# Kernel tuning notes

Hardware: AMD Instinct MI355X
Metric: run time of the kernel (lower is better)

## Reference

```python
import jax, jax.numpy as jnp
import numpy as np

P = 100000   # num places
T = 100000   # num transitions
E = 400000   # edges per direction
H = 128      # hidden_dim
L = 3        # num_gnn_layers


def setup_inputs() -> dict:
    key = jax.random.key(0)
    ks = jax.random.split(key, 24)
    w = lambda i, sh: jax.random.normal(ks[i], sh, dtype=jnp.float32) * 0.02
    z = lambda sh: jnp.zeros(sh, dtype=jnp.float32)
    return {
        "place_features": jax.random.uniform(ks[0], (P,), dtype=jnp.float32),
        "transition_features": jax.random.normal(ks[1], (T, 8), dtype=jnp.float32),
        "prefix_encoding": jax.random.normal(ks[2], (18,), dtype=jnp.float32),
        # pre edges: place -> transition ; post edges: transition -> place
        "pre_edge_index": jnp.stack([jax.random.randint(ks[3], (E,), 0, P),
                                     jax.random.randint(ks[4], (E,), 0, T)]).astype(jnp.int32),
        "post_edge_index": jnp.stack([jax.random.randint(ks[5], (E,), 0, T),
                                      jax.random.randint(ks[6], (E,), 0, P)]).astype(jnp.int32),
        # embeddings
        "W_pe": w(7, (1, H)), "b_pe": z((H,)),
        "W_te": w(8, (8, H)), "b_te": z((H,)),
        "W_pr": w(9, (18, H)), "b_pr": z((H,)),
        # per-layer HeteroGraphConv params (stacked over L)
        "p2t_W": w(10, (L, H, H)), "p2t_b": z((L, H)),
        "t2p_W": w(11, (L, H, H)), "t2p_b": z((L, H)),
        "pu_W": w(12, (L, 2 * H, H)), "pu_b": z((L, H)),
        "tu_W": w(13, (L, 2 * H, H)), "tu_b": z((L, H)),
        "pa_W": w(14, (L, H)), "pa_b": z((L,)),
        "ta_W": w(15, (L, H)), "ta_b": z((L,)),
        # pooling + predictor head
        "W_pp": w(16, (H, H)), "b_pp": z((H,)),
        "W_tp": w(17, (H, H)), "b_tp": z((H,)),
        "W1": w(18, (3 * H, 2 * H)), "b1": z((2 * H,)),
        "W2": w(19, (2 * H, H)), "b2": z((H,)),
        "W3": w(20, (H, T)), "b3": z((T,)),
    }


def _forward(place_features, transition_features, prefix_encoding,
             W_pe, b_pe, W_te, b_te, W_pr, b_pr,
             p2t_W, p2t_b, t2p_W, t2p_b, pu_W, pu_b, tu_W, tu_b,
             pa_W, pa_b, ta_W, ta_b,
             W_pp, b_pp, W_tp, b_tp, W1, b1, W2, b2, W3, b3,
             pre_edge_index, post_edge_index):
    place_h = place_features[:, None] @ W_pe + b_pe            # [P,H]
    trans_h = transition_features @ W_te + b_te                # [T,H]
    prefix_h = prefix_encoding[None, :] @ W_pr + b_pr          # [1,H]
    p_src, p_dst = pre_edge_index[0], pre_edge_index[1]        # place idx, trans idx
    t_src, t_dst = post_edge_index[0], post_edge_index[1]      # trans idx, place idx
    nP, nT = place_h.shape[0], trans_h.shape[0]
    for l in range(L):  # fixed small layer count
        # place -> transition: gather, linear, softmax over ALL edges (dim=0 in torch), scatter-add
        m_pt = place_h[p_src] @ p2t_W[l] + p2t_b[l]            # [E,H]
        a_pt = jax.nn.softmax(m_pt @ ta_W[l] + ta_b[l], axis=0)  # [E]
        trans_msg = jax.ops.segment_sum(m_pt * a_pt[:, None], p_dst, num_segments=nT)
        # transition -> place
        m_tp = trans_h[t_src] @ t2p_W[l] + t2p_b[l]            # [E,H]
        a_tp = jax.nn.softmax(m_tp @ pa_W[l] + pa_b[l], axis=0)
        place_msg = jax.ops.segment_sum(m_tp * a_tp[:, None], t_dst, num_segments=nP)
        # residual update + relu (dropout is identity at eval)
        place_new = jnp.concatenate([place_h, place_msg], axis=1) @ pu_W[l] + pu_b[l]
        trans_new = jnp.concatenate([trans_h, trans_msg], axis=1) @ tu_W[l] + tu_b[l]
        place_h = jax.nn.relu(place_h + place_new)
        trans_h = jax.nn.relu(trans_h + trans_new)
    place_global = jnp.mean(place_h @ W_pp + b_pp, axis=0, keepdims=True)   # [1,H]
    trans_global = jnp.mean(trans_h @ W_tp + b_tp, axis=0, keepdims=True)   # [1,H]
    combined = jnp.concatenate([place_global, trans_global, prefix_h], axis=1)  # [1,3H]
    h1 = jax.nn.relu(combined @ W1 + b1)
    h2 = jax.nn.relu(h1 @ W2 + b2)
    logits = h2 @ W3 + b3                                      # [1,T]
    return jax.nn.sigmoid(logits)                              # predicted_transitions


def reference(place_features, transition_features, prefix_encoding,
              pre_edge_index, post_edge_index,
              W_pe, b_pe, W_te, b_te, W_pr, b_pr,
              p2t_W, p2t_b, t2p_W, t2p_b, pu_W, pu_b, tu_W, tu_b,
              pa_W, pa_b, ta_W, ta_b,
              W_pp, b_pp, W_tp, b_tp, W1, b1, W2, b2, W3, b3):
    return _forward(place_features, transition_features, prefix_encoding,
                    W_pe, b_pe, W_te, b_te, W_pr, b_pr,
                    p2t_W, p2t_b, t2p_W, t2p_b, pu_W, pu_b, tu_W, tu_b,
                    pa_W, pa_b, ta_W, ta_b,
                    W_pp, b_pp, W_tp, b_tp, W1, b1, W2, b2, W3, b3,
                    pre_edge_index, post_edge_index)
```

## Files before the change

### kernel.cpp

```cpp
#include <hip/hip_runtime.h>
#include <cstddef>

#define H 128

typedef unsigned short ushort_t;
typedef unsigned char uchar_t;
typedef __attribute__((ext_vector_type(8))) short short8;
typedef __attribute__((ext_vector_type(4))) float floatx4;
typedef __attribute__((ext_vector_type(2))) float floatx2;

__device__ __forceinline__ unsigned fkey(float f){
    unsigned u = __float_as_uint(f);
    return (u & 0x80000000u) ? ~u : (u | 0x80000000u);
}
__device__ __forceinline__ float funkey(unsigned k){
    unsigned u = (k & 0x80000000u) ? (k ^ 0x80000000u) : ~k;
    return __uint_as_float(u);
}
__device__ __forceinline__ ushort_t f2bf(float f){
    unsigned u = __float_as_uint(f);
    u += 0x7fffu + ((u >> 16) & 1u);
    return (ushort_t)(u >> 16);
}
__device__ __forceinline__ float bf2f(ushort_t h){
    return __uint_as_float(((unsigned)h) << 16);
}
__device__ __forceinline__ uchar_t f2fp8(float v){
    int p = __builtin_amdgcn_cvt_pk_fp8_f32(v, v, 0, false);
    return (uchar_t)(p & 0xff);
}
__device__ __forceinline__ void gll16(const void* g, void* l){
    __builtin_amdgcn_global_load_lds(
        (const __attribute__((address_space(1))) unsigned int*)g,
        (__attribute__((address_space(3))) unsigned int*)l, 16, 0, 0);
}
__device__ __forceinline__ void acc8f8(float* a, int2 u, float w){
    floatx2 p;
    p = __builtin_amdgcn_cvt_pk_f32_fp8(u.x, false); a[0] += w*p.x; a[1] += w*p.y;
    p = __builtin_amdgcn_cvt_pk_f32_fp8(u.x, true);  a[2] += w*p.x; a[3] += w*p.y;
    p = __builtin_amdgcn_cvt_pk_f32_fp8(u.y, false); a[4] += w*p.x; a[5] += w*p.y;
    p = __builtin_amdgcn_cvt_pk_f32_fp8(u.y, true);  a[6] += w*p.x; a[7] += w*p.y;
}

__global__ __launch_bounds__(256) void k_embed_place(
    const float* __restrict__ pf, const float* __restrict__ Wpe,
    const float* __restrict__ bpe, ushort_t* __restrict__ out,
    uchar_t* __restrict__ outf8, int P)
{
    int idx = blockIdx.x*256 + threadIdx.x;
    if (idx >= P*32) return;
    int p = idx >> 5, q = (idx & 31) << 2;
    float v = pf[p];
    float4 w = *(const float4*)(Wpe + q);
    float4 b = *(const float4*)(bpe + q);
    float v0 = v*w.x + b.x, v1 = v*w.y + b.y, v2 = v*w.z + b.z, v3 = v*w.w + b.w;
    ushort4 o;
    o.x = f2bf(v0); o.y = f2bf(v1); o.z = f2bf(v2); o.w = f2bf(v3);
    *(ushort4*)(out + (size_t)p*H + q) = o;
    int pk = __builtin_amdgcn_cvt_pk_fp8_f32(v0, v1, 0, false);
    pk = __builtin_amdgcn_cvt_pk_fp8_f32(v2, v3, pk, true);
    *(int*)(outf8 + (size_t)p*H + q) = pk;
}

__global__ __launch_bounds__(256) void k_embed_trans(
    const float* __restrict__ tf, const float* __restrict__ Wte,
    const float* __restrict__ bte, ushort_t* __restrict__ out,
    uchar_t* __restrict__ outf8, int T)
{
    __shared__ float Wl[8*H];
    __shared__ float Bl[H];
    int tid = threadIdx.x;
    #pragma unroll
    for (int t = 0; t < 4; t++) Wl[tid + t*256] = Wte[tid + t*256];
    if (tid < H) Bl[tid] = bte[tid];
    __syncthreads();
    int idx = blockIdx.x*256 + tid;
    if (idx >= T*32) return;
    int t = idx >> 5, q = (idx & 31) << 2;
    float4 acc = *(float4*)(&Bl[q]);
    #pragma unroll
    for (int k = 0; k < 8; k++){
        float s = tf[(size_t)t*8 + k];
        float4 w = *(float4*)(&Wl[k*H + q]);
        acc.x += s*w.x; acc.y += s*w.y; acc.z += s*w.z; acc.w += s*w.w;
    }
    ushort4 o;
    o.x = f2bf(acc.x); o.y = f2bf(acc.y); o.z = f2bf(acc.z); o.w = f2bf(acc.w);
    *(ushort4*)(out + (size_t)t*H + q) = o;
    int pk = __builtin_amdgcn_cvt_pk_fp8_f32(acc.x, acc.y, 0, false);
    pk = __builtin_amdgcn_cvt_pk_fp8_f32(acc.z, acc.w, pk, true);
    *(int*)(outf8 + (size_t)t*H + q) = pk;
}

__global__ void k_init_small(const float* __restrict__ pe, int plen,
                             const float* __restrict__ Wpr, const float* __restrict__ bpr,
                             float* __restrict__ prefix, float* __restrict__ meanP,
                             float* __restrict__ meanT, float* __restrict__ slots)
{
    int c = threadIdx.x;
    float a = bpr[c];
    for (int k = 0; k < plen; k++) a += pe[k]*Wpr[k*H + c];
    prefix[c] = a;
    meanP[c] = 0.f;
    meanT[c] = 0.f;
    if (c < 16) slots[c] = 0.f;
}

__global__ __launch_bounds__(256) void k_wconv(
    const float* __restrict__ tu_W, const float* __restrict__ pu_W,
    ushort_t* __restrict__ WT, int total)
{
    int e = blockIdx.x*256 + threadIdx.x;
    if (e >= total) return;
    int l = e / 32768, oo = e - l*32768;
    int side = oo >> 14, o2 = oo & 16383;
    int n = o2 >> 7, k = o2 & 127;
    const float* Bm = side ? (pu_W + (size_t)l*32768) : (tu_W + (size_t)l*32768);
    WT[(size_t)l*65536 + (size_t)side*32768 + n*256 + k] = f2bf(Bm[(size_t)k*H + n]);
}

__global__ __launch_bounds__(256) void k_wfold(
    const float* __restrict__ p2t_W, const float* __restrict__ t2p_W,
    const float* __restrict__ tu_W,  const float* __restrict__ pu_W,
    ushort_t* __restrict__ WT, int total)
{
    int e = blockIdx.x*256 + threadIdx.x;
    if (e >= total) return;
    int l = e / 32768, oo = e - l*32768;
    int side = oo >> 14, o2 = oo & 16383;
    int n = o2 >> 7, k = o2 & 127;
    const float* A  = side ? (t2p_W + (size_t)l*16384) : (p2t_W + (size_t)l*16384);
    const float* Bm = side ? (pu_W  + (size_t)l*32768) : (tu_W  + (size_t)l*32768);
    const float* Ar = A + (size_t)k*H;
    const float* Bc = Bm + (size_t)128*H + n;
    float s = 0.f;
    #pragma unroll 4
    for (int j = 0; j < 128; j++) s += Ar[j] * Bc[(size_t)j*H];
    WT[(size_t)l*65536 + (size_t)side*32768 + n*256 + 128 + k] = f2bf(s);
}

__global__ __launch_bounds__(128) void k_wsmall(
    const float* __restrict__ p2t_W, const float* __restrict__ t2p_W,
    const float* __restrict__ tu_W,  const float* __restrict__ pu_W,
    const float* __restrict__ p2t_b, const float* __restrict__ t2p_b,
    const float* __restrict__ ta_W,  const float* __restrict__ ta_b,
    const float* __restrict__ pa_W,  const float* __restrict__ pa_b,
    float* __restrict__ wv, float* __restrict__ c0v, float* __restrict__ bcv)
{
    int b = blockIdx.x, l = b >> 1, side = b & 1;
    const float* A  = side ? (t2p_W + (size_t)l*16384) : (p2t_W + (size_t)l*16384);
    const float* Bm = side ? (pu_W  + (size_t)l*32768) : (tu_W  + (size_t)l*32768);
    const float* ab = side ? (t2p_b + (size_t)l*H) : (p2t_b + (size_t)l*H);
    const float* av = side ? (pa_W  + (size_t)l*H) : (ta_W  + (size_t)l*H);
    float asc       = side ? pa_b[l] : ta_b[l];
    int tid = threadIdx.x;
    int o = (l*2 + side)*H;
    float s = 0.f;
    for (int n = 0; n < 128; n++) s += A[(size_t)tid*H + n] * av[n];
    wv[o + tid] = s;
    float s2 = 0.f;
    for (int j = 0; j < 128; j++) s2 += ab[j] * Bm[(size_t)(128+j)*H + tid];
    bcv[o + tid] = s2;
    if (tid == 0){
        float c = 0.f;
        for (int n = 0; n < 128; n++) c += ab[n]*av[n];
        c0v[l*2 + side] = c + asc;
    }
}

__global__ __launch_bounds__(256) void k_zero_ints(int* __restrict__ p, int n)
{
    int i = blockIdx.x*256 + threadIdx.x;
    int stride = gridDim.x*256;
    for (; i < n; i += stride) p[i] = 0;
}

__global__ __launch_bounds__(256) void k_hist2(
    const int* __restrict__ preD, const int* __restrict__ postD, int E,
    int* __restrict__ cntPre, int* __restrict__ cntPost,
    int* __restrict__ rankPre, int* __restrict__ rankPost)
{
    int i = blockIdx.x*256 + threadIdx.x;
    int stride = gridDim.x*256;
    for (; i < E; i += stride){
        rankPre[i] = atomicAdd(&cntPre[preD[i]], 1);
        rankPost[i] = atomicAdd(&cntPost[postD[i]], 1);
    }
}

__global__ __launch_bounds__(256) void k_scan_part(
    const int* __restrict__ cnt, int N, int* __restrict__ bsum)
{
    __shared__ int wsum[4];
    int tid = threadIdx.x, lane = tid & 63, wid = tid >> 6;
    int base = blockIdx.x*1024 + tid*4;
    int4 v = make_int4(0,0,0,0);
    if (base + 3 < N) v = *(const int4*)(cnt + base);
    else {
        if (base+0 < N) v.x = cnt[base+0];
        if (base+1 < N) v.y = cnt[base+1];
        if (base+2 < N) v.z = cnt[base+2];
    }
    int s = v.x + v.y + v.z + v.w;
    #pragma unroll
    for (int o = 1; o < 64; o <<= 1) s += __shfl_xor(s, o);
    if (lane == 0) wsum[wid] = s;
    __syncthreads();
    if (tid == 0) bsum[blockIdx.x] = wsum[0] + wsum[1] + wsum[2] + wsum[3];
}

__global__ __launch_bounds__(256) void k_scan_bsum(int* __restrict__ bsum, int nb)
{
    __shared__ int wsum[4];
    int tid = threadIdx.x, lane = tid & 63, wid = tid >> 6;
    int x = (tid < nb) ? bsum[tid] : 0;
    int inc = x;
    #pragma unroll
    for (int o = 1; o < 64; o <<= 1){
        int u = __shfl_up(inc, o);
        if (lane >= o) inc += u;
    }
    if (lane == 63) wsum[wid] = inc;
    __syncthreads();
    int woff = 0;
    if (wid > 0) woff += wsum[0];
    if (wid > 1) woff += wsum[1];
    if (wid > 2) woff += wsum[2];
    if (tid < nb) bsum[tid] = woff + inc - x;
}

__global__ __launch_bounds__(256) void k_scan_final(
    const int* __restrict__ cnt, int N, const int* __restrict__ bsum,
    int* __restrict__ rp, int E)
{
    __shared__ int wsum[4];
    int tid = threadIdx.x, lane = tid & 63, wid = tid >> 6;
    int base = blockIdx.x*1024 + tid*4;
    int4 v = make_int4(0,0,0,0);
    if (base + 3 < N) v = *(const int4*)(cnt + base);
    else {
        if (base+0 < N) v.x = cnt[base+0];
        if (base+1 < N) v.y = cnt[base+1];
        if (base+2 < N) v.z = cnt[base+2];
    }
    int t0 = v.x, t1 = t0 + v.y, t2 = t1 + v.z, t3 = t2 + v.w;
    int inc = t3;
    #pragma unroll
    for (int o = 1; o < 64; o <<= 1){
        int u = __shfl_up(inc, o);
        if (lane >= o) inc += u;
    }
    if (lane == 63) wsum[wid] = inc;
    __syncthreads();
    int woff = 0;
    if (wid > 0) woff += wsum[0];
    if (wid > 1) woff += wsum[1];
    if (wid > 2) woff += wsum[2];
    int off = bsum[blockIdx.x] + woff + inc - t3;
    if (base+0 < N) rp[base+0] = off;
    if (base+1 < N) rp[base+1] = off + t0;
    if (base+2 < N) rp[base+2] = off + t1;
    if (base+3 < N) rp[base+3] = off + t2;
    if (blockIdx.x == 0 && tid == 0) rp[N] = E;
}

__global__ __launch_bounds__(256) void k_fill2(
    const int* __restrict__ preS, const int* __restrict__ preD,
    const int* __restrict__ postS, const int* __restrict__ postD, int E,
    const int* __restrict__ rpPre, const int* __restrict__ rankPre, int* __restrict__ csrPre,
    const int* __restrict__ rpPost, const int* __restrict__ rankPost, int* __restrict__ csrPost)
{
    int i = blockIdx.x*256 + threadIdx.x;
    int stride = gridDim.x*256;
    for (; i < E; i += stride){
        csrPre[rpPre[preD[i]] + rankPre[i]] = preS[i];
        csrPost[rpPost[postD[i]] + rankPost[i]] = postS[i];
    }
}

__global__ __launch_bounds__(256) void k_gemv(
    const ushort_t* __restrict__ A, int M,
    const float* __restrict__ wv, const float* __restrict__ c0v, int c0i,
    float* __restrict__ y, unsigned* __restrict__ Mkey)
{
    __shared__ float wm[4];
    int tid = threadIdx.x, lane = tid & 63, wid = tid >> 6;
    int g = tid >> 4, gl = tid & 15;
    float w8[8];
    #pragma unroll
    for (int i = 0; i < 8; i++) w8[i] = wv[gl*8 + i];
    float c0 = c0v[c0i];
    int stride = gridDim.x*16;
    float lmax = -3.402823466e38f;
    for (int r = blockIdx.x*16 + g; r < M; r += stride){
        short8 u = *(const short8*)(A + (size_t)r*H + gl*8);
        float s = 0.f;
        #pragma unroll
        for (int i = 0; i < 8; i++) s += bf2f((ushort_t)u[i]) * w8[i];
        s += __shfl_xor(s, 1); s += __shfl_xor(s, 2);
        s += __shfl_xor(s, 4); s += __shfl_xor(s, 8);
        s += c0;
        if (gl == 0) y[r] = s;
        lmax = fmaxf(lmax, s);
    }
    #pragma unroll
    for (int o = 1; o < 64; o <<= 1) lmax = fmaxf(lmax, __shfl_xor(lmax, o));
    if (lane == 0) wm[wid] = lmax;
    __syncthreads();
    if (tid == 0){
        float m = fmaxf(fmaxf(wm[0], wm[1]), fmaxf(wm[2], wm[3]));
        atomicMax(Mkey, fkey(m));
    }
}

__global__ __launch_bounds__(256) void k_sumexp(
    const int* __restrict__ src, int E, const float* __restrict__ y,
    const unsigned* __restrict__ Mkey, float* __restrict__ Sp)
{
    __shared__ float red[4];
    int tid = threadIdx.x, lane = tid & 63, wid = tid >> 6;
    int gid = blockIdx.x*256 + tid, stride = gridDim.x*256;
    float Mv = funkey(Mkey[0]);
    float ls = 0.f;
    for (int e = gid; e < E; e += stride) ls += expf(y[src[e]] - Mv);
    #pragma unroll
    for (int o = 1; o < 64; o <<= 1) ls += __shfl_xor(ls, o);
    if (lane == 0) red[wid] = ls;
    __syncthreads();
    if (tid == 0) atomicAdd(Sp, red[0] + red[1] + red[2] + red[3]);
}

__global__ __launch_bounds__(256) void k_gatherH(
    const int* __restrict__ rp, const int* __restrict__ csr, int Nrow,
    const float* __restrict__ y, const uchar_t* __restrict__ X,
    ushort_t* __restrict__ G, float* __restrict__ sdeg,
    const unsigned* __restrict__ Mkey)
{
    int tid = threadIdx.x;
    int g = tid >> 4, gl = tid & 15;
    int r = blockIdx.x*16 + g;
    if (r >= Nrow) return;
    float Mv = funkey(Mkey[0]);
    int j0 = rp[r], j1 = rp[r+1];
    const int2* X8 = (const int2*)X;
    float a[8] = {0.f,0.f,0.f,0.f,0.f,0.f,0.f,0.f};
    float se = 0.f;
    int j = j0;
    for (; j + 1 < j1; j += 2){
        int s0 = csr[j], s1 = csr[j+1];
        float e0 = expf(y[s0] - Mv);
        float e1 = expf(y[s1] - Mv);
        int2 u0 = X8[(size_t)s0*16 + gl];
        int2 u1 = X8[(size_t)s1*16 + gl];
        se += e0 + e1;
        acc8f8(a, u0, e0);
        acc8f8(a, u1, e1);
    }
    if (j < j1){
        int s0 = csr[j];
        float e0 = expf(y[s0] - Mv);
        int2 u0 = X8[(size_t)s0*16 + gl];
        se += e0;
        acc8f8(a, u0, e0);
    }
    int4 o;
    o.x = (int)((((unsigned)f2bf(a[1])) << 16) | (unsigned)f2bf(a[0]));
    o.y = (int)((((unsigned)f2bf(a[3])) << 16) | (unsigned)f2bf(a[2]));
    o.z = (int)((((unsigned)f2bf(a[5])) << 16) | (unsigned)f2bf(a[4]));
    o.w = (int)((((unsigned)f2bf(a[7])) << 16) | (unsigned)f2bf(a[6]));
    ((int4*)G)[(size_t)r*16 + gl] = o;
    if (gl == 0) sdeg[r] = se;
}

__global__ __launch_bounds__(256, 4) void k_gemm_up(
    const ushort_t* A1, const ushort_t* __restrict__ A2,
    const ushort_t* __restrict__ WT, const float* __restrict__ bias,
    const float* __restrict__ bcp, const float* __restrict__ Sp,
    const float* __restrict__ sdeg,
    ushort_t* out, uchar_t* __restrict__ outF8, int M,
    float* __restrict__ colsum)
{
    __shared__ __align__(16) char As[3*8192];
    __shared__ float csum[H];
    int tid = threadIdx.x;
    int lane = tid & 63, wid = tid >> 6;
    int quad = lane >> 4, l15 = lane & 15;
    int strip = wid*32;
    short8 bfr1[2][4], bfr2[2][4];
    float bcol[2], bc2[2];
    #pragma unroll
    for (int j = 0; j < 2; j++){
        int col = strip + j*16 + l15;
        #pragma unroll
        for (int kk = 0; kk < 4; kk++){
            bfr1[j][kk] = *(const short8*)(WT + (size_t)col*256 + kk*32 + quad*8);
            bfr2[j][kk] = *(const short8*)(WT + (size_t)col*256 + 128 + kk*32 + quad*8);
        }
        bcol[j] = bias[col];
        bc2[j]  = bcp[col];
    }
    short8 If0, If1;
    #pragma unroll
    for (int e = 0; e < 8; e++){
        int kloc = quad*8 + e;
        If0[e] = (kloc == l15)      ? (short)0x3F80 : (short)0;
        If1[e] = (kloc == l15 + 16) ? (short)0x3F80 : (short)0;
    }
    float invS = 1.f / Sp[0];
    const bool has_cs = (colsum != nullptr);
    if (has_cs && tid < H) csum[tid] = 0.f;
    float cs[2] = {0.f, 0.f};

    int tiles = (M + 15) >> 4;
    int G = gridDim.x;
    int t0 = blockIdx.x;
    if (t0 >= tiles) return;
    int srow = tid >> 4;
    int su = (tid & 15) ^ srow;
    const ushort_t* g1b = A1 + (size_t)srow*H + su*8;
    const ushort_t* g2b = A2 + (size_t)srow*H + su*8;
    char* AsB = As;

    #define STAGE_UP(bo, t) do { \
        gll16(g1b + (size_t)(t)*(16*H), AsB + (bo) + (wid<<10)); \
        gll16(g2b + (size_t)(t)*(16*H), AsB + (bo) + 4096 + (wid<<10)); \
    } while(0)

    STAGE_UP(0, t0);
    int t1p = t0 + G;
    if (t1p < tiles){
        STAGE_UP(8192, t1p);
        asm volatile("s_waitcnt vmcnt(2)\ns_barrier" ::: "memory");
    } else {
        asm volatile("s_waitcnt vmcnt(0)\ns_barrier" ::: "memory");
    }

    int t = t0, bo = 0;
    for (;;){
        const char* rb = AsB + bo;
        int row0 = t << 4;
        float4 sd4 = *(const float4*)(sdeg + row0 + quad*4);
        float sdv[4] = {sd4.x, sd4.y, sd4.z, sd4.w};
        short8 a1f[4], a2f[4];
        #pragma unroll
        for (int kk = 0; kk < 4; kk++){
            int sw = ((((kk<<2)+quad) ^ l15) << 4);
            a1f[kk] = *(const short8*)(rb + (l15<<8) + sw);
            a2f[kk] = *(const short8*)(rb + 4096 + (l15<<8) + sw);
        }
        short8 ares = *(const short8*)(rb + (l15<<8) + ((((wid<<2)+quad) ^ l15) << 4));
        floatx4 acc1[2], acc2[2];
        acc1[0] = __builtin_amdgcn_mfma_f32_16x16x32_bf16(ares, If0, (floatx4)0.f, 0,0,0);
        acc1[1] = __builtin_amdgcn_mfma_f32_16x16x32_bf16(ares, If1, (floatx4)0.f, 0,0,0);
        acc2[0] = (floatx4)0.f; acc2[1] = (floatx4)0.f;
        #pragma unroll
        for (int j = 0; j < 2; j++){
            #pragma unroll
            for (int kk = 0; kk < 4; kk++)
                acc1[j] = __builtin_amdgcn_mfma_f32_16x16x32_bf16(a1f[kk], bfr1[j][kk], acc1[j], 0,0,0);
            #pragma unroll
            for (int kk = 0; kk < 4; kk++)
                acc2[j] = __builtin_amdgcn_mfma_f32_16x16x32_bf16(a2f[kk], bfr2[j][kk], acc2[j], 0,0,0);
        }
        #pragma unroll
        for (int j = 0; j < 2; j++){
            int col = strip + j*16 + l15;
            #pragma unroll
            for (int rr = 0; rr < 4; rr++){
                int grow = row0 + quad*4 + rr;
                float v = acc1[j][rr] + invS*(acc2[j][rr] + sdv[rr]*bc2[j]) + bcol[j];
                v = fmaxf(v, 0.f);
                out[(size_t)grow*H + col] = f2bf(v);
                outF8[(size_t)grow*H + col] = f2fp8(v);
                if (has_cs) cs[j] += v;
            }
        }
        int tn = t + G;
        if (tn >= tiles) break;
        int tnn = tn + G;
        int bo2 = bo + 8192; if (bo2 >= 24576) bo2 = 0;
        int bo3 = bo2 + 8192; if (bo3 >= 24576) bo3 = 0;
        if (tnn < tiles){
            STAGE_UP(bo3, tnn);
            asm volatile("s_waitcnt vmcnt(19)\ns_barrier" ::: "memory");
        } else {
            asm volatile("s_waitcnt vmcnt(17)\ns_barrier" ::: "memory");
        }
        t = tn; bo = bo2;
    }
    #undef STAGE_UP
    if (has_cs){
        #pragma unroll
        for (int j = 0; j < 2; j++){
            float v = cs[j];
            v += __shfl_xor(v, 16); v += __shfl_xor(v, 32);
            if (quad == 0) atomicAdd(&csum[strip + j*16 + l15], v);
        }
        __syncthreads();
        if (tid < H) atomicAdd(&colsum[tid], csum[tid]);
    }
}

__global__ __launch_bounds__(256) void k_head(
    const float* __restrict__ meanP, const float* __restrict__ meanT,
    float invP, float invT,
    const float* __restrict__ Wpp, const float* __restrict__ bpp,
    const float* __restrict__ Wtp, const float* __restrict__ btp,
    const float* __restrict__ prefix,
    const float* __restrict__ W1, const float* __restrict__ b1,
    const float* __restrict__ W2, const float* __restrict__ b2,
    float* __restrict__ h2g)
{
    __shared__ float comb[384];
    __shared__ float h1s[256];
    int tid = threadIdx.x;
    if (tid < 128){
        float a = bpp[tid];
        for (int k = 0; k < 128; k++) a += meanP[k]*invP*Wpp[k*H + tid];
        comb[tid] = a;
        comb[256 + tid] = prefix[tid];
    } else {
        int c = tid - 128;
        float a = btp[c];
        for (int k = 0; k < 128; k++) a += meanT[k]*invT*Wtp[k*H + c];
        comb[128 + c] = a;
    }
    __syncthreads();
    {
        float a = b1[tid];
        for (int k = 0; k < 384; k++) a += comb[k]*W1[k*256 + tid];
        h1s[tid] = fmaxf(a, 0.f);
    }
    __syncthreads();
    if (tid < 128){
        float a = b2[tid];
        for (int k = 0; k < 256; k++) a += h1s[k]*W2[k*H + tid];
        h2g[tid] = fmaxf(a, 0.f);
    }
}

__global__ __launch_bounds__(256) void k_logits(
    const float* __restrict__ h2g, const float* __restrict__ W3,
    const float* __restrict__ b3, float* __restrict__ out, int T)
{
    __shared__ float h2l[128];
    int tid = threadIdx.x;
    if (tid < 128) h2l[tid] = h2g[tid];
    __syncthreads();
    int t = blockIdx.x*256 + tid;
    if (t >= T) return;
    float a = b3[t];
    #pragma unroll 8
    for (int k = 0; k < 128; k++) a += h2l[k]*W3[(size_t)k*T + t];
    out[t] = 1.f/(1.f + expf(-a));
}

extern "C" void kernel_launch(void* const* d_in, const int* in_sizes, int n_in,
                              void* d_out, int out_size, void* d_ws, size_t ws_size,
                              hipStream_t stream)
{
    (void)n_in; (void)out_size; (void)ws_size;
    const float* pf    = (const float*)d_in[0];
    const float* tf    = (const float*)d_in[1];
    const float* pe    = (const float*)d_in[2];
    const int*   pre   = (const int*)d_in[3];
    const int*   post  = (const int*)d_in[4];
    const float* W_pe  = (const float*)d_in[5];
    const float* b_pe  = (const float*)d_in[6];
    const float* W_te  = (const float*)d_in[7];
    const float* b_te  = (const float*)d_in[8];
    const float* W_pr  = (const float*)d_in[9];
    const float* b_pr  = (const float*)d_in[10];
    const float* p2t_W = (const float*)d_in[11];
    const float* p2t_b = (const float*)d_in[12];
    const float* t2p_W = (const float*)d_in[13];
    const float* t2p_b = (const float*)d_in[14];
    const float* pu_W  = (const float*)d_in[15];
    const float* pu_b  = (const float*)d_in[16];
    const float* tu_W  = (const float*)d_in[17];
    const float* tu_b  = (const float*)d_in[18];
    const float* pa_W  = (const float*)d_in[19];
    const float* pa_b  = (const float*)d_in[20];
    const float* ta_W  = (const float*)d_in[21];
    const float* ta_b  = (const float*)d_in[22];
    const float* W_pp  = (const float*)d_in[23];
    const float* b_pp  = (const float*)d_in[24];
    const float* W_tp  = (const float*)d_in[25];
    const float* b_tp  = (const float*)d_in[26];
    const float* W1    = (const float*)d_in[27];
    const float* b1    = (const float*)d_in[28];
    const float* W2    = (const float*)d_in[29];
    const float* b2    = (const float*)d_in[30];
    const float* W3    = (const float*)d_in[31];
    const float* b3    = (const float*)d_in[32];

    int P = in_sizes[0];
    int T = in_sizes[1] / 8;
    int E = in_sizes[3] / 2;
    int plen = in_sizes[2];
    int L = in_sizes[11] / (H*H);

    float* ws = (float*)d_ws;
    size_t fP = (size_t)P*H, fT = (size_t)T*H;
    size_t fN = (fP > fT) ? fP : fT;
    int   Nmax = (P > T) ? P : T;

    float* yb    = ws;
    float* sdegA = yb + Nmax;
    float* sdegB = sdegA + Nmax;
    float* sc    = sdegB + Nmax;
    float* meanP   = sc + 16;
    float* meanT   = sc + 144;
    float* prefix  = sc + 272;
    float* h2g     = sc + 400;
    float* wvv  = sc + 544;
    float* c0v  = wvv + (size_t)L*256;
    float* bcv  = c0v + 32;

    ushort_t* bh = (ushort_t*)(bcv + (size_t)L*256);
    ushort_t* place_h = bh;
    ushort_t* trans_h = place_h + fP;
    ushort_t* GbA     = trans_h + fT;
    ushort_t* GbB     = GbA + fN;
    ushort_t* WTb     = GbB + fN;
    uchar_t*  XP      = (uchar_t*)(WTb + (size_t)L*65536);
    uchar_t*  XT      = XP + fP;

    int* iw = (int*)(XT + fT);
    int* cntPre  = iw;
    int* cntPost = cntPre + T;
    int* rpPre   = cntPost + P;
    int* rpPost  = rpPre + (T + 1);
    int* csrPre  = rpPost + (P + 2);
    int* csrPost = csrPre + E;
    int* rankPre = csrPost + E;
    int* rankPost= rankPre + E;
    int* bsumA   = rankPost + E;
    int* bsumB   = bsumA + 256;

    const int* pre_src  = pre;          const int* pre_dst  = pre + E;
    const int* post_src = post;         const int* post_dst = post + E;

    int wtot = L*32768;
    int nbT = (T + 1023)/1024, nbP = (P + 1023)/1024;

    int tilesP = (P + 15) >> 4, tilesT = (T + 15) >> 4;
    int gridP = (tilesP + 4)/5, gridT = (tilesT + 4)/5;

    k_init_small<<<1, 128, 0, stream>>>(pe, plen, W_pr, b_pr, prefix, meanP, meanT, sc);
    k_wconv<<<(wtot + 255)/256, 256, 0, stream>>>(tu_W, pu_W, WTb, wtot);
    k_wfold<<<(wtot + 255)/256, 256, 0, stream>>>(p2t_W, t2p_W, tu_W, pu_W, WTb, wtot);
    k_wsmall<<<L*2, 128, 0, stream>>>(p2t_W, t2p_W, tu_W, pu_W, p2t_b, t2p_b,
                                      ta_W, ta_b, pa_W, pa_b, wvv, c0v, bcv);
    k_zero_ints<<<256, 256, 0, stream>>>(iw, P + T);
    k_hist2<<<2048, 256, 0, stream>>>(pre_dst, post_dst, E,
                                      cntPre, cntPost, rankPre, rankPost);
    k_scan_part<<<nbT, 256, 0, stream>>>(cntPre, T, bsumA);
    k_scan_bsum<<<1, 256, 0, stream>>>(bsumA, nbT);
    k_scan_final<<<nbT, 256, 0, stream>>>(cntPre, T, bsumA, rpPre, E);
    k_scan_part<<<nbP, 256, 0, stream>>>(cntPost, P, bsumB);
    k_scan_bsum<<<1, 256, 0, stream>>>(bsumB, nbP);
    k_scan_final<<<nbP, 256, 0, stream>>>(cntPost, P, bsumB, rpPost, E);
    k_fill2<<<1024, 256, 0, stream>>>(pre_src, pre_dst, post_src, post_dst, E,
                                      rpPre, rankPre, csrPre,
                                      rpPost, rankPost, csrPost);

    k_embed_place<<<(P*32 + 255)/256, 256, 0, stream>>>(pf, W_pe, b_pe, place_h, XP, P);
    k_embed_trans<<<(T*32 + 255)/256, 256, 0, stream>>>(tf, W_te, b_te, trans_h, XT, T);

    for (int l = 0; l < L; l++){
        const ushort_t* tuT = WTb + (size_t)l*65536;
        const ushort_t* puT = tuT + 32768;
        const float* pub  = pu_b  + (size_t)l*H;
        const float* tub  = tu_b  + (size_t)l*H;
        const float* wvA  = wvv + (size_t)(l*2 + 0)*H;
        const float* wvB  = wvv + (size_t)(l*2 + 1)*H;
        const float* bcA  = bcv + (size_t)(l*2 + 0)*H;
        const float* bcB  = bcv + (size_t)(l*2 + 1)*H;
        unsigned* MkA = (unsigned*)(sc + l*4 + 0);   float* SpA = sc + l*4 + 1;
        unsigned* MkB = (unsigned*)(sc + l*4 + 2);   float* SpB = sc + l*4 + 3;
        int last = (l == L-1);

        k_gemv<<<512, 256, 0, stream>>>(place_h, P, wvA, c0v, l*2 + 0, yb, MkA);
        k_sumexp<<<256, 256, 0, stream>>>(pre_src, E, yb, MkA, SpA);
        k_gatherH<<<(T + 15)/16, 256, 0, stream>>>(rpPre, csrPre, T, yb, XP,
                                                   GbA, sdegA, MkA);
        k_gemv<<<512, 256, 0, stream>>>(trans_h, T, wvB, c0v, l*2 + 1, yb, MkB);
        k_sumexp<<<256, 256, 0, stream>>>(post_src, E, yb, MkB, SpB);
        k_gatherH<<<(P + 15)/16, 256, 0, stream>>>(rpPost, csrPost, P, yb, XT,
                                                   GbB, sdegB, MkB);

        k_gemm_up<<<gridT, 256, 0, stream>>>(trans_h, GbA, tuT, tub, bcA, SpA,
                                             sdegA, trans_h, XT, T,
                                             last ? meanT : nullptr);
        k_gemm_up<<<gridP, 256, 0, stream>>>(place_h, GbB, puT, pub, bcB, SpB,
                                             sdegB, place_h, XP, P,
                                             last ? meanP : nullptr);
    }

    k_head<<<1, 256, 0, stream>>>(meanP, meanT, 1.f/(float)P, 1.f/(float)T,
                                  W_pp, b_pp, W_tp, b_tp, prefix, W1, b1, W2, b2, h2g);
    k_logits<<<(T + 255)/256, 256, 0, stream>>>(h2g, W3, b3, (float*)d_out, T);
}
```

Before: 771.1 us.

## Merge place/transition passes per layer into combined kernels and precompute edge weights

Each layer's gemv, sum-exp, gather and update kernels for the place and transition sides are merged into single launches that split blocks between the two sides, halving launch count and improving occupancy. Edge softmax weights are computed once in CSR order and stored, so the gather reads them instead of recomputing exp and indirectly loading y. The last layer skips storing hidden states and only accumulates column sums, through a template specialization with adjusted waitcnt values. This needs separate y buffers for each side and reuses rank arrays as edge-weight storage.

```diff
diff --git a/kernel.cpp b/kernel.cpp
--- a/kernel.cpp
+++ b/kernel.cpp
@@ -278,21 +278,33 @@
     }
 }
 
-__global__ __launch_bounds__(256) void k_gemv(
-    const ushort_t* __restrict__ A, int M,
-    const float* __restrict__ wv, const float* __restrict__ c0v, int c0i,
-    float* __restrict__ y, unsigned* __restrict__ Mkey)
+__global__ __launch_bounds__(256) void k_gemv2(
+    const ushort_t* __restrict__ Ap, int P,
+    const ushort_t* __restrict__ At, int T,
+    const float* __restrict__ wvA, const float* __restrict__ wvB,
+    const float* __restrict__ c0v, int c0iA, int c0iB,
+    float* __restrict__ yA, float* __restrict__ yB,
+    unsigned* __restrict__ MkA, unsigned* __restrict__ MkB)
 {
     __shared__ float wm[4];
+    int half = gridDim.x >> 1;
+    int side = (blockIdx.x >= half);
+    const ushort_t* A = side ? At : Ap;
+    int M = side ? T : P;
+    const float* wv = side ? wvB : wvA;
+    float c0 = c0v[side ? c0iB : c0iA];
+    float* y = side ? yB : yA;
+    unsigned* Mk = side ? MkB : MkA;
+    int b = side ? (blockIdx.x - half) : blockIdx.x;
+
     int tid = threadIdx.x, lane = tid & 63, wid = tid >> 6;
     int g = tid >> 4, gl = tid & 15;
     float w8[8];
     #pragma unroll
     for (int i = 0; i < 8; i++) w8[i] = wv[gl*8 + i];
-    float c0 = c0v[c0i];
-    int stride = gridDim.x*16;
+    int stride = half*16;
     float lmax = -3.402823466e38f;
-    for (int r = blockIdx.x*16 + g; r < M; r += stride){
+    for (int r = b*16 + g; r < M; r += stride){
         short8 u = *(const short8*)(A + (size_t)r*H + gl*8);
         float s = 0.f;
         #pragma unroll
@@ -309,20 +321,35 @@
     __syncthreads();
     if (tid == 0){
         float m = fmaxf(fmaxf(wm[0], wm[1]), fmaxf(wm[2], wm[3]));
-        atomicMax(Mkey, fkey(m));
-    }
-}
-
-__global__ __launch_bounds__(256) void k_sumexp(
-    const int* __restrict__ src, int E, const float* __restrict__ y,
-    const unsigned* __restrict__ Mkey, float* __restrict__ Sp)
+        atomicMax(Mk, fkey(m));
+    }
+}
+
+__global__ __launch_bounds__(256) void k_ew2(
+    const int* __restrict__ csrPre, const int* __restrict__ csrPost, int E,
+    const float* __restrict__ yA, const float* __restrict__ yB,
+    const unsigned* __restrict__ MkA, const unsigned* __restrict__ MkB,
+    float* __restrict__ ewA, float* __restrict__ ewB,
+    float* __restrict__ SpA, float* __restrict__ SpB)
 {
     __shared__ float red[4];
+    int half = gridDim.x >> 1;
+    int side = (blockIdx.x >= half);
+    const int* csr = side ? csrPost : csrPre;
+    const float* y = side ? yB : yA;
+    float Mv = funkey((side ? MkB : MkA)[0]);
+    float* ew = side ? ewB : ewA;
+    float* Sp = side ? SpB : SpA;
+    int b = side ? (blockIdx.x - half) : blockIdx.x;
+
     int tid = threadIdx.x, lane = tid & 63, wid = tid >> 6;
-    int gid = blockIdx.x*256 + tid, stride = gridDim.x*256;
-    float Mv = funkey(Mkey[0]);
+    int gid = b*256 + tid, stride = half*256;
     float ls = 0.f;
-    for (int e = gid; e < E; e += stride) ls += expf(y[src[e]] - Mv);
+    for (int j = gid; j < E; j += stride){
+        float w = expf(y[csr[j]] - Mv);
+        ew[j] = w;
+        ls += w;
+    }
     #pragma unroll
     for (int o = 1; o < 64; o <<= 1) ls += __shfl_xor(ls, o);
     if (lane == 0) red[wid] = ls;
@@ -330,17 +357,29 @@
     if (tid == 0) atomicAdd(Sp, red[0] + red[1] + red[2] + red[3]);
 }
 
-__global__ __launch_bounds__(256) void k_gatherH(
-    const int* __restrict__ rp, const int* __restrict__ csr, int Nrow,
-    const float* __restrict__ y, const uchar_t* __restrict__ X,
-    ushort_t* __restrict__ G, float* __restrict__ sdeg,
-    const unsigned* __restrict__ Mkey)
-{
+__global__ __launch_bounds__(256) void k_gather2(
+    const int* __restrict__ rpPre, const int* __restrict__ csrPre, int T,
+    const int* __restrict__ rpPost, const int* __restrict__ csrPost, int P,
+    const float* __restrict__ ewA, const float* __restrict__ ewB,
+    const uchar_t* __restrict__ XP, const uchar_t* __restrict__ XT,
+    ushort_t* __restrict__ GbA, ushort_t* __restrict__ GbB,
+    float* __restrict__ sdegA, float* __restrict__ sdegB)
+{
+    int nbT = (T + 15) >> 4;
+    int side = (blockIdx.x >= nbT);
+    const int* rp   = side ? rpPost : rpPre;
+    const int* csr  = side ? csrPost : csrPre;
+    const float* ew = side ? ewB : ewA;
+    const uchar_t* X = side ? XT : XP;
+    ushort_t* G     = side ? GbB : GbA;
+    float* sdeg     = side ? sdegB : sdegA;
+    int Nrow        = side ? P : T;
+    int b = side ? (blockIdx.x - nbT) : blockIdx.x;
+
     int tid = threadIdx.x;
     int g = tid >> 4, gl = tid & 15;
-    int r = blockIdx.x*16 + g;
+    int r = b*16 + g;
     if (r >= Nrow) return;
-    float Mv = funkey(Mkey[0]);
     int j0 = rp[r], j1 = rp[r+1];
     const int2* X8 = (const int2*)X;
     float a[8] = {0.f,0.f,0.f,0.f,0.f,0.f,0.f,0.f};
@@ -348,8 +387,7 @@
     int j = j0;
     for (; j + 1 < j1; j += 2){
         int s0 = csr[j], s1 = csr[j+1];
-        float e0 = expf(y[s0] - Mv);
-        float e1 = expf(y[s1] - Mv);
+        float e0 = ew[j], e1 = ew[j+1];
         int2 u0 = X8[(size_t)s0*16 + gl];
         int2 u1 = X8[(size_t)s1*16 + gl];
         se += e0 + e1;
@@ -358,7 +396,7 @@
     }
     if (j < j1){
         int s0 = csr[j];
-        float e0 = expf(y[s0] - Mv);
+        float e0 = ew[j];
         int2 u0 = X8[(size_t)s0*16 + gl];
         se += e0;
         acc8f8(a, u0, e0);
@@ -372,16 +410,35 @@
     if (gl == 0) sdeg[r] = se;
 }
 
-__global__ __launch_bounds__(256, 4) void k_gemm_up(
-    const ushort_t* A1, const ushort_t* __restrict__ A2,
-    const ushort_t* __restrict__ WT, const float* __restrict__ bias,
-    const float* __restrict__ bcp, const float* __restrict__ Sp,
-    const float* __restrict__ sdeg,
-    ushort_t* out, uchar_t* __restrict__ outF8, int M,
-    float* __restrict__ colsum)
+template<bool STORE>
+__global__ __launch_bounds__(256, 4) void k_up2(
+    ushort_t* trans_h, ushort_t* place_h,
+    const ushort_t* __restrict__ GbA, const ushort_t* __restrict__ GbB,
+    const ushort_t* __restrict__ WTl,
+    const float* __restrict__ tub, const float* __restrict__ pub,
+    const float* __restrict__ bcA, const float* __restrict__ bcB,
+    const float* __restrict__ sc4,
+    const float* __restrict__ sdegA, const float* __restrict__ sdegB,
+    uchar_t* __restrict__ XT, uchar_t* __restrict__ XP,
+    int T, int P, int gridT, int gridP,
+    float* __restrict__ meanT, float* __restrict__ meanP)
 {
     __shared__ __align__(16) char As[3*8192];
     __shared__ float csum[H];
+    int side = (blockIdx.x >= gridT);
+    ushort_t* A1        = side ? place_h : trans_h;
+    const ushort_t* A2  = side ? GbB : GbA;
+    const ushort_t* WT  = WTl + (side ? 32768 : 0);
+    const float* bias   = side ? pub : tub;
+    const float* bcp    = side ? bcB : bcA;
+    const float* sdeg   = side ? sdegB : sdegA;
+    uchar_t* outF8      = side ? XP : XT;
+    int M               = side ? P : T;
+    int G               = side ? gridP : gridT;
+    int t0              = side ? (blockIdx.x - gridT) : blockIdx.x;
+    float* colsum       = side ? meanP : meanT;
+    float invS = 1.f / (side ? sc4[3] : sc4[1]);
+
     int tid = threadIdx.x;
     int lane = tid & 63, wid = tid >> 6;
     int quad = lane >> 4, l15 = lane & 15;
@@ -406,14 +463,10 @@
         If0[e] = (kloc == l15)      ? (short)0x3F80 : (short)0;
         If1[e] = (kloc == l15 + 16) ? (short)0x3F80 : (short)0;
     }
-    float invS = 1.f / Sp[0];
-    const bool has_cs = (colsum != nullptr);
-    if (has_cs && tid < H) csum[tid] = 0.f;
+    if constexpr (!STORE){ if (tid < H) csum[tid] = 0.f; }
     float cs[2] = {0.f, 0.f};
 
     int tiles = (M + 15) >> 4;
-    int G = gridDim.x;
-    int t0 = blockIdx.x;
     if (t0 >= tiles) return;
     int srow = tid >> 4;
     int su = (tid & 15) ^ srow;
@@ -470,9 +523,12 @@
                 int grow = row0 + quad*4 + rr;
                 float v = acc1[j][rr] + invS*(acc2[j][rr] + sdv[rr]*bc2[j]) + bcol[j];
                 v = fmaxf(v, 0.f);
-                out[(size_t)grow*H + col] = f2bf(v);
-                outF8[(size_t)grow*H + col] = f2fp8(v);
-                if (has_cs) cs[j] += v;
+                if constexpr (STORE){
+                    A1[(size_t)grow*H + col] = f2bf(v);
+                    outF8[(size_t)grow*H + col] = f2fp8(v);
+                } else {
+                    cs[j] += v;
+                }
             }
         }
         int tn = t + G;
@@ -482,14 +538,16 @@
         int bo3 = bo2 + 8192; if (bo3 >= 24576) bo3 = 0;
         if (tnn < tiles){
             STAGE_UP(bo3, tnn);
-            asm volatile("s_waitcnt vmcnt(19)\ns_barrier" ::: "memory");
+            if constexpr (STORE) asm volatile("s_waitcnt vmcnt(19)\ns_barrier" ::: "memory");
+            else                 asm volatile("s_waitcnt vmcnt(3)\ns_barrier" ::: "memory");
         } else {
-            asm volatile("s_waitcnt vmcnt(17)\ns_barrier" ::: "memory");
+            if constexpr (STORE) asm volatile("s_waitcnt vmcnt(17)\ns_barrier" ::: "memory");
+            else                 asm volatile("s_waitcnt vmcnt(1)\ns_barrier" ::: "memory");
         }
         t = tn; bo = bo2;
     }
     #undef STAGE_UP
-    if (has_cs){
+    if constexpr (!STORE){
         #pragma unroll
         for (int j = 0; j < 2; j++){
             float v = cs[j];
@@ -605,8 +663,9 @@
     size_t fN = (fP > fT) ? fP : fT;
     int   Nmax = (P > T) ? P : T;
 
-    float* yb    = ws;
-    float* sdegA = yb + Nmax;
+    float* yA    = ws;
+    float* yB    = yA + Nmax;
+    float* sdegA = yB + Nmax;
     float* sdegB = sdegA + Nmax;
     float* sc    = sdegB + Nmax;
     float* meanP   = sc + 16;
@@ -638,6 +697,9 @@
     int* bsumA   = rankPost + E;
     int* bsumB   = bsumA + 256;
 
+    float* ewA = (float*)rankPre;
+    float* ewB = (float*)rankPost;
+
     const int* pre_src  = pre;          const int* pre_dst  = pre + E;
     const int* post_src = post;         const int* post_dst = post + E;
 
@@ -646,6 +708,7 @@
 
     int tilesP = (P + 15) >> 4, tilesT = (T + 15) >> 4;
     int gridP = (tilesP + 4)/5, gridT = (tilesT + 4)/5;
+    int nbTg = (T + 15) >> 4, nbPg = (P + 15) >> 4;
 
     k_init_small<<<1, 128, 0, stream>>>(pe, plen, W_pr, b_pr, prefix, meanP, meanT, sc);
     k_wconv<<<(wtot + 255)/256, 256, 0, stream>>>(tu_W, pu_W, WTb, wtot);
@@ -669,8 +732,7 @@
     k_embed_trans<<<(T*32 + 255)/256, 256, 0, stream>>>(tf, W_te, b_te, trans_h, XT, T);
 
     for (int l = 0; l < L; l++){
-        const ushort_t* tuT = WTb + (size_t)l*65536;
-        const ushort_t* puT = tuT + 32768;
+        const ushort_t* WTl = WTb + (size_t)l*65536;
         const float* pub  = pu_b  + (size_t)l*H;
         const float* tub  = tu_b  + (size_t)l*H;
         const float* wvA  = wvv + (size_t)(l*2 + 0)*H;
@@ -681,21 +743,22 @@
         unsigned* MkB = (unsigned*)(sc + l*4 + 2);   float* SpB = sc + l*4 + 3;
         int last = (l == L-1);
 
-        k_gemv<<<512, 256, 0, stream>>>(place_h, P, wvA, c0v, l*2 + 0, yb, MkA);
-        k_sumexp<<<256, 256, 0, stream>>>(pre_src, E, yb, MkA, SpA);
-        k_gatherH<<<(T + 15)/16, 256, 0, stream>>>(rpPre, csrPre, T, yb, XP,
-                                                   GbA, sdegA, MkA);
-        k_gemv<<<512, 256, 0, stream>>>(trans_h, T, wvB, c0v, l*2 + 1, yb, MkB);
-        k_sumexp<<<256, 256, 0, stream>>>(post_src, E, yb, MkB, SpB);
-        k_gatherH<<<(P + 15)/16, 256, 0, stream>>>(rpPost, csrPost, P, yb, XT,
-                                                   GbB, sdegB, MkB);
-
-        k_gemm_up<<<gridT, 256, 0, stream>>>(trans_h, GbA, tuT, tub, bcA, SpA,
-                                             sdegA, trans_h, XT, T,
-                                             last ? meanT : nullptr);
-        k_gemm_up<<<gridP, 256, 0, stream>>>(place_h, GbB, puT, pub, bcB, SpB,
-                                             sdegB, place_h, XP, P,
-                                             last ? meanP : nullptr);
+        k_gemv2<<<1024, 256, 0, stream>>>(place_h, P, trans_h, T, wvA, wvB,
+                                          c0v, l*2 + 0, l*2 + 1, yA, yB, MkA, MkB);
+        k_ew2<<<1024, 256, 0, stream>>>(csrPre, csrPost, E, yA, yB, MkA, MkB,
+                                        ewA, ewB, SpA, SpB);
+        k_gather2<<<nbTg + nbPg, 256, 0, stream>>>(rpPre, csrPre, T,
+                                                   rpPost, csrPost, P,
+                                                   ewA, ewB, XP, XT,
+                                                   GbA, GbB, sdegA, sdegB);
+        if (last)
+            k_up2<false><<<gridT + gridP, 256, 0, stream>>>(
+                trans_h, place_h, GbA, GbB, WTl, tub, pub, bcA, bcB,
+                sc + l*4, sdegA, sdegB, XT, XP, T, P, gridT, gridP, meanT, meanP);
+        else
+            k_up2<true><<<gridT + gridP, 256, 0, stream>>>(
+                trans_h, place_h, GbA, GbB, WTl, tub, pub, bcA, bcB,
+                sc + l*4, sdegA, sdegB, XT, XP, T, P, gridT, gridP, meanT, meanP);
     }
 
     k_head<<<1, 256, 0, stream>>>(meanP, meanT, 1.f/(float)P, 1.f/(float)T,
```

Result: faster. 684.3 us (-11.3%).
